# Kernel tuning notes

Hardware: AMD Instinct MI355X
Metric: run time of the kernel (lower is better)

The kernel has to match this reference:

```python
import jax, jax.numpy as jnp
import numpy as np

DIM = 768
HEADS = 12
HEAD_DIM = DIM // HEADS
EPS = 1e-5


def layernorm(x, gamma, beta):
    mu = jnp.mean(x, axis=-1, keepdims=True)
    var = jnp.var(x, axis=-1, keepdims=True)
    return (x - mu) * jax.lax.rsqrt(var + EPS) * gamma + beta


def setup_inputs() -> dict:
    key = jax.random.key(0)
    ks = jax.random.split(key, 9)
    B, N, C = 4, 2048, DIM
    s_in = 1.0 / np.sqrt(C)
    return {
        "x": jax.random.normal(ks[0], (B, N, C), dtype=jnp.float32),
        "qkv_w": jax.random.normal(ks[1], (3 * C, C), dtype=jnp.float32) * s_in,
        "qkv_b": jnp.zeros((3 * C,), dtype=jnp.float32),
        "proj_w": jax.random.normal(ks[2], (C, C), dtype=jnp.float32) * s_in,
        "proj_b": jnp.zeros((C,), dtype=jnp.float32),
        "q_gamma": jnp.ones((HEAD_DIM,), dtype=jnp.float32),
        "q_beta": jnp.zeros((HEAD_DIM,), dtype=jnp.float32),
        "k_gamma": jnp.ones((HEAD_DIM,), dtype=jnp.float32),
        "k_beta": jnp.zeros((HEAD_DIM,), dtype=jnp.float32),
    }


def reference(x, qkv_w, qkv_b, proj_w, proj_b, q_gamma, q_beta, k_gamma, k_beta):
    B, N, C = x.shape
    H, Dh = HEADS, C // HEADS
    scale = Dh ** (-0.5)
    # qkv projection: [B,N,3C] -> [3,B,H,N,Dh]
    qkv = (x @ qkv_w.T + qkv_b).reshape(B, N, 3, H, Dh).transpose(2, 0, 3, 1, 4)
    q, k, v = qkv[0], qkv[1], qkv[2]
    q = layernorm(q, q_gamma, q_beta)
    k = layernorm(k, k_gamma, k_beta)
    # explicit full score matrix [B,H,N,N] as in the original module
    attn = jnp.einsum("bhqd,bhkd->bhqk", q, k) * scale
    attn = jax.nn.softmax(attn, axis=-1)
    out = jnp.einsum("bhqk,bhkd->bhqd", attn, v)  # [B,H,N,Dh]
    out = out.transpose(0, 2, 1, 3).reshape(B, N, C)
    return out @ proj_w.T + proj_b
```

## Files before the change

### kernel.cpp

```cpp
#include <hip/hip_runtime.h>
#include <hip/hip_bf16.h>
#include <cstdint>
#include <cstddef>

#define BB 4
#define SEQ 2048
#define CD 768
#define NH 12
#define DH 64
#define MROWS (BB*SEQ)
#define NQKV (3*CD)

typedef float f32x4 __attribute__((ext_vector_type(4)));
typedef float f32x16 __attribute__((ext_vector_type(16)));
typedef short bf16x8 __attribute__((ext_vector_type(8)));

static __device__ __forceinline__ unsigned short f2bf(float f) {
  union { float f; unsigned int u; } cv; cv.f = f;
  unsigned int u = cv.u;
  unsigned int r = (u + 0x7FFFu + ((u >> 16) & 1u)) >> 16;
  return (unsigned short)r;
}

static __device__ __forceinline__ float fexp2(float x) {
#if __has_builtin(__builtin_amdgcn_exp2f)
  return __builtin_amdgcn_exp2f(x);
#else
  float r; asm("v_exp_f32 %0, %1" : "=v"(r) : "v"(x)); return r;
#endif
}

#define GAS __attribute__((address_space(1)))
#define LAS __attribute__((address_space(3)))
static __device__ __forceinline__ void gl2lds16(const void* g, void* l) {
  __builtin_amdgcn_global_load_lds((const GAS void*)g, (LAS void*)l, 16, 0, 0);
}

#define MFMA(a, b, c) __builtin_amdgcn_mfma_f32_16x16x32_bf16((a), (b), (c), 0, 0, 0)
#define MFMA32(a, b, c) __builtin_amdgcn_mfma_f32_32x32x16_bf16((a), (b), (c), 0, 0, 0)
#define PACKBF(dst, x, y) asm("v_cvt_pk_bf16_f32 %0, %1, %2" : "=v"(dst) : "v"(x), "v"(y))
#define SWAP32(a, b) asm("v_permlane32_swap_b32 %0, %1" : "+v"(a), "+v"(b))

#define QSC 0.18033688011112042f

__global__ __launch_bounds__(256) void cvt_bf16(const float* __restrict__ in,
                                                unsigned short* __restrict__ out, int n4) {
  int i = blockIdx.x * 256 + threadIdx.x;
  if (i >= n4) return;
  float4 v = reinterpret_cast<const float4*>(in)[i];
  unsigned int lo = (unsigned int)f2bf(v.x) | ((unsigned int)f2bf(v.y) << 16);
  unsigned int hi = (unsigned int)f2bf(v.z) | ((unsigned int)f2bf(v.w) << 16);
  reinterpret_cast<uint2*>(out)[i] = make_uint2(lo, hi);
}

__global__ __launch_bounds__(256) void qkv_gemm(
    const unsigned short* __restrict__ Xb, const unsigned short* __restrict__ Wb,
    const float* __restrict__ bias,
    const float* __restrict__ qg, const float* __restrict__ qbt,
    const float* __restrict__ kg, const float* __restrict__ kbt,
    unsigned short* __restrict__ Qo, unsigned short* __restrict__ Ko,
    unsigned short* __restrict__ Vt) {
  __shared__ unsigned short Als[2][128 * 64];
  __shared__ unsigned short Bls[2][128 * 64];
  const int tid = threadIdx.x;
  const int wid = tid >> 6, lane = tid & 63;
  const int g = lane >> 4, cl = lane & 15;
  const int wr = (wid >> 1) * 64, wc = (wid & 1) * 64;

  const int wg = blockIdx.x;
  const int wgid = (wg & 7) * 144 + (wg >> 3);
  const int bm = wgid / 18, bn = wgid % 18;

  f32x4 acc[4][4] = {};

  const int srow = tid >> 3;
  const int scol = ((tid & 7) ^ (srow & 7)) * 8;
  const unsigned short* Abase = Xb + (size_t)(bm * 128 + srow) * CD + scol;
  const unsigned short* Bbase = Wb + (size_t)(bn * 128 + srow) * CD + scol;

#define QSTG(buf, kt)                                                         \
  do {                                                                        \
    gl2lds16(Abase + (size_t)0 * 32 * CD + (kt) * 64, &Als[buf][0 * 2048 + tid * 8]); \
    gl2lds16(Abase + (size_t)1 * 32 * CD + (kt) * 64, &Als[buf][1 * 2048 + tid * 8]); \
    gl2lds16(Abase + (size_t)2 * 32 * CD + (kt) * 64, &Als[buf][2 * 2048 + tid * 8]); \
    gl2lds16(Abase + (size_t)3 * 32 * CD + (kt) * 64, &Als[buf][3 * 2048 + tid * 8]); \
    gl2lds16(Bbase + (size_t)0 * 32 * CD + (kt) * 64, &Bls[buf][0 * 2048 + tid * 8]); \
    gl2lds16(Bbase + (size_t)1 * 32 * CD + (kt) * 64, &Bls[buf][1 * 2048 + tid * 8]); \
    gl2lds16(Bbase + (size_t)2 * 32 * CD + (kt) * 64, &Bls[buf][2 * 2048 + tid * 8]); \
    gl2lds16(Bbase + (size_t)3 * 32 * CD + (kt) * 64, &Bls[buf][3 * 2048 + tid * 8]); \
  } while (0)

  QSTG(0, 0);
  __syncthreads();
  const int NKT = CD / 64;
  for (int kt = 0; kt < NKT; ++kt) {
    const int cur = kt & 1;
    if (kt + 1 < NKT) QSTG(cur ^ 1, kt + 1);
    bf16x8 bfr[4][2];
#pragma unroll
    for (int j = 0; j < 4; ++j) {
      const int Bcol = wc + j * 16 + cl;
      const int sw = (Bcol & 7) << 3;
      bfr[j][0] = *(const bf16x8*)&Bls[cur][Bcol * 64 + ((g * 8) ^ sw)];
      bfr[j][1] = *(const bf16x8*)&Bls[cur][Bcol * 64 + ((32 + g * 8) ^ sw)];
    }
    __builtin_amdgcn_s_setprio(1);
#pragma unroll
    for (int i = 0; i < 4; ++i) {
      const int Arow = wr + i * 16 + cl;
      const int sw = (Arow & 7) << 3;
      bf16x8 a0 = *(const bf16x8*)&Als[cur][Arow * 64 + ((g * 8) ^ sw)];
      bf16x8 a1 = *(const bf16x8*)&Als[cur][Arow * 64 + ((32 + g * 8) ^ sw)];
#pragma unroll
      for (int j = 0; j < 4; ++j) {
        acc[i][j] = MFMA(a0, bfr[j][0], acc[i][j]);
        acc[i][j] = MFMA(a1, bfr[j][1], acc[i][j]);
      }
    }
    __builtin_amdgcn_s_setprio(0);
    __syncthreads();
  }
#undef QSTG

  const int j0 = bn * 128 + wc;
  const int t = j0 / CD;
  const int h = (j0 % CD) / DH;
  float bia[4], gam[4] = {0, 0, 0, 0}, bet[4] = {0, 0, 0, 0};
#pragma unroll
  for (int j = 0; j < 4; ++j) {
    int d = j * 16 + cl;
    bia[j] = bias[j0 + d];
    if (t == 0) { gam[j] = qg[d] * QSC; bet[j] = qbt[d] * QSC; }
    else if (t == 1) { gam[j] = kg[d]; bet[j] = kbt[d]; }
  }

  if (t == 2) {
#pragma unroll
    for (int i = 0; i < 4; ++i) {
      const int mrow = bm * 128 + wr + i * 16 + g * 4;
      const int b = mrow >> 11, nn = mrow & 2047;
#pragma unroll
      for (int j = 0; j < 4; ++j) {
        const int d = j * 16 + cl;
        unsigned int lo = (unsigned int)f2bf(acc[i][j][0] + bia[j]) |
                          ((unsigned int)f2bf(acc[i][j][1] + bia[j]) << 16);
        unsigned int hi2 = (unsigned int)f2bf(acc[i][j][2] + bia[j]) |
                           ((unsigned int)f2bf(acc[i][j][3] + bia[j]) << 16);
        *reinterpret_cast<uint2*>(&Vt[((size_t)(b * NH + h) * DH + d) * SEQ + nn]) =
            make_uint2(lo, hi2);
      }
    }
    return;
  }

  unsigned short* Out = (t == 0) ? Qo : Ko;
#pragma unroll
  for (int i = 0; i < 4; ++i) {
#pragma unroll
    for (int r = 0; r < 4; ++r) {
      float vj[4];
#pragma unroll
      for (int j = 0; j < 4; ++j) vj[j] = acc[i][j][r] + bia[j];
      const int m = bm * 128 + wr + i * 16 + g * 4 + r;
      const int b = m >> 11, n = m & 2047;
      size_t base = ((size_t)(b * NH + h) * SEQ + n) * DH;
      float s = vj[0] + vj[1] + vj[2] + vj[3];
      float ss = vj[0] * vj[0] + vj[1] * vj[1] + vj[2] * vj[2] + vj[3] * vj[3];
#pragma unroll
      for (int msk = 1; msk < 16; msk <<= 1) {
        s += __shfl_xor(s, msk, 64);
        ss += __shfl_xor(ss, msk, 64);
      }
      float mu = s * (1.0f / 64.0f);
      float var = ss * (1.0f / 64.0f) - mu * mu;
      float rstd = rsqrtf(var + 1e-5f);
#pragma unroll
      for (int j = 0; j < 4; ++j)
        Out[base + j * 16 + cl] = f2bf((vj[j] - mu) * rstd * gam[j] + bet[j]);
    }
  }
}

__global__ __launch_bounds__(256, 3) void attn_fwd(
    const unsigned short* __restrict__ Qb, const unsigned short* __restrict__ Kb,
    const unsigned short* __restrict__ Vtb, unsigned short* __restrict__ Ob) {
  __shared__ unsigned short kl[2][64 * 64];
  __shared__ unsigned short vt[2][64 * 64];
  __shared__ float linv[4][32];
  const int tid = threadIdx.x, wave = tid >> 6, lane = tid & 63;
  const int q32 = lane & 31, hi = lane >> 5;

  const int wg = blockIdx.x;
  const int lin = (wg & 7) * 96 + (wg >> 3);
  const int bh = lin >> 4;
  const int qbase = (lin & 15) * 128 + wave * 32;

  const unsigned short* qrow = Qb + ((size_t)bh * SEQ + qbase + q32) * DH + hi * 8;
  bf16x8 qf[4];
#pragma unroll
  for (int dc = 0; dc < 4; ++dc) qf[dc] = *(const bf16x8*)&qrow[dc * 16];

  const unsigned short* Kh = Kb + (size_t)bh * SEQ * DH;
  const unsigned short* Vth = Vtb + (size_t)bh * DH * SEQ;

  const int sr = tid >> 3;
  const int sc = 8 * ((tid & 7) ^ (sr & 7));
  const int ksw = (q32 & 7) << 3;

#define ASTAGE(buf, kb0)                                                      \
  do {                                                                        \
    gl2lds16(&Kh[(size_t)((kb0) + sr) * DH + sc], &kl[buf][tid * 8]);         \
    gl2lds16(&Kh[(size_t)((kb0) + sr + 32) * DH + sc], &kl[buf][tid * 8 + 2048]); \
    gl2lds16(&Vth[(size_t)sr * SEQ + (kb0) + sc], &vt[buf][tid * 8]);         \
    gl2lds16(&Vth[(size_t)(sr + 32) * SEQ + (kb0) + sc], &vt[buf][tid * 8 + 2048]); \
  } while (0)

  f32x16 o0 = {}, o1 = {};
  float su0 = 0.0f, su1 = 0.0f, su2 = 0.0f, su3 = 0.0f;

  ASTAGE(0, 0);
  __syncthreads();
  const int NT = SEQ / 64;
#pragma unroll 2
  for (int it = 0; it < NT; ++it) {
    const int cur = it & 1;
    if (it + 1 < NT) ASTAGE(cur ^ 1, (it + 1) * 64);

    f32x16 s0 = {}, s1 = {};
    __builtin_amdgcn_s_setprio(1);
#pragma unroll
    for (int dc = 0; dc < 4; ++dc) {
      const int colb = dc * 16 + hi * 8;
      bf16x8 kf0 = *(const bf16x8*)&kl[cur][q32 * 64 + (colb ^ ksw)];
      bf16x8 kf1 = *(const bf16x8*)&kl[cur][(32 + q32) * 64 + (colb ^ ksw)];
      s0 = MFMA32(kf0, qf[dc], s0);
      s1 = MFMA32(kf1, qf[dc], s1);
    }
    __builtin_amdgcn_s_setprio(0);

#pragma unroll
    for (int r = 0; r < 16; r += 4) {
      s0[r + 0] = fexp2(s0[r + 0]); su0 += s0[r + 0];
      s0[r + 1] = fexp2(s0[r + 1]); su1 += s0[r + 1];
      s0[r + 2] = fexp2(s0[r + 2]); su2 += s0[r + 2];
      s0[r + 3] = fexp2(s0[r + 3]); su3 += s0[r + 3];
    }
#pragma unroll
    for (int r = 0; r < 16; r += 4) {
      s1[r + 0] = fexp2(s1[r + 0]); su0 += s1[r + 0];
      s1[r + 1] = fexp2(s1[r + 1]); su1 += s1[r + 1];
      s1[r + 2] = fexp2(s1[r + 2]); su2 += s1[r + 2];
      s1[r + 3] = fexp2(s1[r + 3]); su3 += s1[r + 3];
    }

    bf16x8 pav[4];
#pragma unroll
    for (int c = 0; c < 4; ++c) {
      const int b = 8 * (c & 1);
      unsigned int wA0, wA1, wB0, wB1;
      if (c < 2) {
        PACKBF(wA0, s0[b + 0], s0[b + 1]); PACKBF(wA1, s0[b + 2], s0[b + 3]);
        PACKBF(wB0, s0[b + 4], s0[b + 5]); PACKBF(wB1, s0[b + 6], s0[b + 7]);
      } else {
        PACKBF(wA0, s1[b + 0], s1[b + 1]); PACKBF(wA1, s1[b + 2], s1[b + 3]);
        PACKBF(wB0, s1[b + 4], s1[b + 5]); PACKBF(wB1, s1[b + 6], s1[b + 7]);
      }
      SWAP32(wA0, wB0);
      SWAP32(wA1, wB1);
      union { unsigned int w[4]; bf16x8 v; } u;
      u.w[0] = wA0; u.w[1] = wA1; u.w[2] = wB0; u.w[3] = wB1;
      pav[c] = u.v;
    }

    __builtin_amdgcn_s_setprio(1);
#pragma unroll
    for (int c = 0; c < 4; ++c) {
      const int colb = c * 16 + hi * 8;
      bf16x8 vf0 = *(const bf16x8*)&vt[cur][q32 * 64 + (colb ^ ksw)];
      bf16x8 vf1 = *(const bf16x8*)&vt[cur][(32 + q32) * 64 + (colb ^ ksw)];
      o0 = MFMA32(pav[c], vf0, o0);
      o1 = MFMA32(pav[c], vf1, o1);
    }
    __builtin_amdgcn_s_setprio(0);
    __syncthreads();
  }
#undef ASTAGE

  float lsum = (su0 + su1) + (su2 + su3);
  lsum += __shfl_xor(lsum, 32, 64);
  linv[wave][q32] = __builtin_amdgcn_rcpf(lsum);
  __syncthreads();

  const int b = bh / NH, h = bh % NH;
#pragma unroll
  for (int r = 0; r < 16; ++r) {
    const int qq = (r & 3) + 8 * (r >> 2) + 4 * hi;
    const float iv = linv[wave][qq];
    size_t base = ((size_t)(b * SEQ + qbase + qq)) * CD + h * DH;
    Ob[base + q32] = f2bf(o0[r] * iv);
    Ob[base + 32 + q32] = f2bf(o1[r] * iv);
  }
}

__global__ __launch_bounds__(256) void proj_gemm(
    const unsigned short* __restrict__ Ab, const unsigned short* __restrict__ Wb,
    const float* __restrict__ bias, float* __restrict__ out) {
  __shared__ unsigned short Als[2][128 * 64];
  __shared__ unsigned short Bls[2][128 * 64];
  const int tid = threadIdx.x;
  const int wid = tid >> 6, lane = tid & 63;
  const int g = lane >> 4, cl = lane & 15;
  const int bm = blockIdx.x, bn = blockIdx.y;
  const int wr = (wid >> 1) * 64, wc = (wid & 1) * 64;

  f32x4 acc[4][4] = {};

  const int srow = tid >> 3;
  const int scol = ((tid & 7) ^ (srow & 7)) * 8;
  const unsigned short* Abase = Ab + (size_t)(bm * 128 + srow) * CD + scol;
  const unsigned short* Bbase = Wb + (size_t)(bn * 128 + srow) * CD + scol;

#define PSTG(buf, kt)                                                         \
  do {                                                                        \
    gl2lds16(Abase + (size_t)0 * 32 * CD + (kt) * 64, &Als[buf][0 * 2048 + tid * 8]); \
    gl2lds16(Abase + (size_t)1 * 32 * CD + (kt) * 64, &Als[buf][1 * 2048 + tid * 8]); \
    gl2lds16(Abase + (size_t)2 * 32 * CD + (kt) * 64, &Als[buf][2 * 2048 + tid * 8]); \
    gl2lds16(Abase + (size_t)3 * 32 * CD + (kt) * 64, &Als[buf][3 * 2048 + tid * 8]); \
    gl2lds16(Bbase + (size_t)0 * 32 * CD + (kt) * 64, &Bls[buf][0 * 2048 + tid * 8]); \
    gl2lds16(Bbase + (size_t)1 * 32 * CD + (kt) * 64, &Bls[buf][1 * 2048 + tid * 8]); \
    gl2lds16(Bbase + (size_t)2 * 32 * CD + (kt) * 64, &Bls[buf][2 * 2048 + tid * 8]); \
    gl2lds16(Bbase + (size_t)3 * 32 * CD + (kt) * 64, &Bls[buf][3 * 2048 + tid * 8]); \
  } while (0)

  PSTG(0, 0);
  __syncthreads();
  const int NKT = CD / 64;
  for (int kt = 0; kt < NKT; ++kt) {
    const int cur = kt & 1;
    if (kt + 1 < NKT) PSTG(cur ^ 1, kt + 1);
    bf16x8 bfr[4][2];
#pragma unroll
    for (int j = 0; j < 4; ++j) {
      const int Bcol = wc + j * 16 + cl;
      const int sw = (Bcol & 7) << 3;
      bfr[j][0] = *(const bf16x8*)&Bls[cur][Bcol * 64 + ((g * 8) ^ sw)];
      bfr[j][1] = *(const bf16x8*)&Bls[cur][Bcol * 64 + ((32 + g * 8) ^ sw)];
    }
    __builtin_amdgcn_s_setprio(1);
#pragma unroll
    for (int i = 0; i < 4; ++i) {
      const int Arow = wr + i * 16 + cl;
      const int sw = (Arow & 7) << 3;
      bf16x8 a0 = *(const bf16x8*)&Als[cur][Arow * 64 + ((g * 8) ^ sw)];
      bf16x8 a1 = *(const bf16x8*)&Als[cur][Arow * 64 + ((32 + g * 8) ^ sw)];
#pragma unroll
      for (int j = 0; j < 4; ++j) {
        acc[i][j] = MFMA(a0, bfr[j][0], acc[i][j]);
        acc[i][j] = MFMA(a1, bfr[j][1], acc[i][j]);
      }
    }
    __builtin_amdgcn_s_setprio(0);
    __syncthreads();
  }
#undef PSTG

  const int j0 = bn * 128 + wc;
  float pb4[4];
#pragma unroll
  for (int j = 0; j < 4; ++j) pb4[j] = bias[j0 + j * 16 + cl];
#pragma unroll
  for (int i = 0; i < 4; ++i) {
#pragma unroll
    for (int r = 0; r < 4; ++r) {
      const int m = bm * 128 + wr + i * 16 + g * 4 + r;
      float* orow = out + (size_t)m * CD + j0;
#pragma unroll
      for (int j = 0; j < 4; ++j) orow[j * 16 + cl] = acc[i][j][r] + pb4[j];
    }
  }
}

extern "C" void kernel_launch(void* const* d_in, const int* in_sizes, int n_in,
                              void* d_out, int out_size, void* d_ws, size_t ws_size,
                              hipStream_t stream) {
  const float* x = (const float*)d_in[0];
  const float* qkv_w = (const float*)d_in[1];
  const float* qkv_b = (const float*)d_in[2];
  const float* proj_w = (const float*)d_in[3];
  const float* proj_b = (const float*)d_in[4];
  const float* q_gamma = (const float*)d_in[5];
  const float* q_beta = (const float*)d_in[6];
  const float* k_gamma = (const float*)d_in[7];
  const float* k_beta = (const float*)d_in[8];
  float* out = (float*)d_out;

  char* w = (char*)d_ws;
  unsigned short* Xb = (unsigned short*)w; w += (size_t)MROWS * CD * 2;
  unsigned short* Wq = (unsigned short*)w; w += (size_t)NQKV * CD * 2;
  unsigned short* Wp = (unsigned short*)w; w += (size_t)CD * CD * 2;
  unsigned short* Qo = (unsigned short*)w; w += (size_t)BB * NH * SEQ * DH * 2;
  unsigned short* Ko = (unsigned short*)w; w += (size_t)BB * NH * SEQ * DH * 2;
  unsigned short* Vt = (unsigned short*)w; w += (size_t)BB * NH * SEQ * DH * 2;
  unsigned short* Ob = (unsigned short*)w; w += (size_t)MROWS * CD * 2;

  cvt_bf16<<<MROWS * CD / 1024, 256, 0, stream>>>(x, Xb, MROWS * CD / 4);
  cvt_bf16<<<NQKV * CD / 1024, 256, 0, stream>>>(qkv_w, Wq, NQKV * CD / 4);
  cvt_bf16<<<CD * CD / 1024, 256, 0, stream>>>(proj_w, Wp, CD * CD / 4);

  qkv_gemm<<<(MROWS / 128) * (NQKV / 128), 256, 0, stream>>>(
      Xb, Wq, qkv_b, q_gamma, q_beta, k_gamma, k_beta, Qo, Ko, Vt);

  attn_fwd<<<SEQ / 128 * BB * NH, 256, 0, stream>>>(Qo, Ko, Vt, Ob);

  proj_gemm<<<dim3(MROWS / 128, CD / 128), 256, 0, stream>>>(Ob, Wp, proj_b, out);
}
```

Measured before the change: 145.2 us.

## Stage QKV GEMM epilogue through LDS for vectorized stores; merge bf16 conversions

The three fp32-to-bf16 conversion launches become one kernel that picks its source by index. The QKV GEMM epilogue now writes the accumulators to a swizzled LDS buffer. Each thread then reads a full 64-wide head row, computes LayerNorm serially and writes 16-byte bf16 stores; V^T is written with 16-byte stores along the sequence dimension. This replaces scattered 2-byte and 8-byte stores and the shuffle reductions, at the cost of an extra LDS round trip, a barrier, and 64-float register arrays per thread.

Result: faster. 133.8 us (-7.9%).

```diff
diff --git a/kernel.cpp b/kernel.cpp
--- a/kernel.cpp
+++ b/kernel.cpp
@@ -43,14 +43,25 @@
 
 #define QSC 0.18033688011112042f
 
-__global__ __launch_bounds__(256) void cvt_bf16(const float* __restrict__ in,
-                                                unsigned short* __restrict__ out, int n4) {
+#define CN1 (MROWS * CD / 4)
+#define CN2 (CN1 + NQKV * CD / 4)
+#define CN3 (CN2 + CD * CD / 4)
+__global__ __launch_bounds__(256) void cvt_all(
+    const float* __restrict__ x, const float* __restrict__ wq, const float* __restrict__ wp,
+    unsigned short* __restrict__ Xb, unsigned short* __restrict__ Wq,
+    unsigned short* __restrict__ Wp) {
   int i = blockIdx.x * 256 + threadIdx.x;
-  if (i >= n4) return;
-  float4 v = reinterpret_cast<const float4*>(in)[i];
+  if (i >= CN3) return;
+  const float* src;
+  unsigned short* dst;
+  int k;
+  if (i < CN1) { src = x; dst = Xb; k = i; }
+  else if (i < CN2) { src = wq; dst = Wq; k = i - CN1; }
+  else { src = wp; dst = Wp; k = i - CN2; }
+  float4 v = reinterpret_cast<const float4*>(src)[k];
   unsigned int lo = (unsigned int)f2bf(v.x) | ((unsigned int)f2bf(v.y) << 16);
   unsigned int hi = (unsigned int)f2bf(v.z) | ((unsigned int)f2bf(v.w) << 16);
-  reinterpret_cast<uint2*>(out)[i] = make_uint2(lo, hi);
+  reinterpret_cast<uint2*>(dst)[k] = make_uint2(lo, hi);
 }
 
 __global__ __launch_bounds__(256) void qkv_gemm(
@@ -60,8 +71,9 @@
     const float* __restrict__ kg, const float* __restrict__ kbt,
     unsigned short* __restrict__ Qo, unsigned short* __restrict__ Ko,
     unsigned short* __restrict__ Vt) {
-  __shared__ unsigned short Als[2][128 * 64];
-  __shared__ unsigned short Bls[2][128 * 64];
+  __shared__ unsigned short smem[4 * 128 * 64];
+#define ALS(buf) (&smem[(buf) * 8192])
+#define BLS(buf) (&smem[16384 + (buf) * 8192])
   const int tid = threadIdx.x;
   const int wid = tid >> 6, lane = tid & 63;
   const int g = lane >> 4, cl = lane & 15;
@@ -80,14 +92,14 @@
 
 #define QSTG(buf, kt)                                                         \
   do {                                                                        \
-    gl2lds16(Abase + (size_t)0 * 32 * CD + (kt) * 64, &Als[buf][0 * 2048 + tid * 8]); \
-    gl2lds16(Abase + (size_t)1 * 32 * CD + (kt) * 64, &Als[buf][1 * 2048 + tid * 8]); \
-    gl2lds16(Abase + (size_t)2 * 32 * CD + (kt) * 64, &Als[buf][2 * 2048 + tid * 8]); \
-    gl2lds16(Abase + (size_t)3 * 32 * CD + (kt) * 64, &Als[buf][3 * 2048 + tid * 8]); \
-    gl2lds16(Bbase + (size_t)0 * 32 * CD + (kt) * 64, &Bls[buf][0 * 2048 + tid * 8]); \
-    gl2lds16(Bbase + (size_t)1 * 32 * CD + (kt) * 64, &Bls[buf][1 * 2048 + tid * 8]); \
-    gl2lds16(Bbase + (size_t)2 * 32 * CD + (kt) * 64, &Bls[buf][2 * 2048 + tid * 8]); \
-    gl2lds16(Bbase + (size_t)3 * 32 * CD + (kt) * 64, &Bls[buf][3 * 2048 + tid * 8]); \
+    gl2lds16(Abase + (size_t)0 * 32 * CD + (kt) * 64, ALS(buf) + 0 * 2048 + tid * 8); \
+    gl2lds16(Abase + (size_t)1 * 32 * CD + (kt) * 64, ALS(buf) + 1 * 2048 + tid * 8); \
+    gl2lds16(Abase + (size_t)2 * 32 * CD + (kt) * 64, ALS(buf) + 2 * 2048 + tid * 8); \
+    gl2lds16(Abase + (size_t)3 * 32 * CD + (kt) * 64, ALS(buf) + 3 * 2048 + tid * 8); \
+    gl2lds16(Bbase + (size_t)0 * 32 * CD + (kt) * 64, BLS(buf) + 0 * 2048 + tid * 8); \
+    gl2lds16(Bbase + (size_t)1 * 32 * CD + (kt) * 64, BLS(buf) + 1 * 2048 + tid * 8); \
+    gl2lds16(Bbase + (size_t)2 * 32 * CD + (kt) * 64, BLS(buf) + 2 * 2048 + tid * 8); \
+    gl2lds16(Bbase + (size_t)3 * 32 * CD + (kt) * 64, BLS(buf) + 3 * 2048 + tid * 8); \
   } while (0)
 
   QSTG(0, 0);
@@ -101,16 +113,16 @@
     for (int j = 0; j < 4; ++j) {
       const int Bcol = wc + j * 16 + cl;
       const int sw = (Bcol & 7) << 3;
-      bfr[j][0] = *(const bf16x8*)&Bls[cur][Bcol * 64 + ((g * 8) ^ sw)];
-      bfr[j][1] = *(const bf16x8*)&Bls[cur][Bcol * 64 + ((32 + g * 8) ^ sw)];
+      bfr[j][0] = *(const bf16x8*)&BLS(cur)[Bcol * 64 + ((g * 8) ^ sw)];
+      bfr[j][1] = *(const bf16x8*)&BLS(cur)[Bcol * 64 + ((32 + g * 8) ^ sw)];
     }
     __builtin_amdgcn_s_setprio(1);
 #pragma unroll
     for (int i = 0; i < 4; ++i) {
       const int Arow = wr + i * 16 + cl;
       const int sw = (Arow & 7) << 3;
-      bf16x8 a0 = *(const bf16x8*)&Als[cur][Arow * 64 + ((g * 8) ^ sw)];
-      bf16x8 a1 = *(const bf16x8*)&Als[cur][Arow * 64 + ((32 + g * 8) ^ sw)];
+      bf16x8 a0 = *(const bf16x8*)&ALS(cur)[Arow * 64 + ((g * 8) ^ sw)];
+      bf16x8 a1 = *(const bf16x8*)&ALS(cur)[Arow * 64 + ((32 + g * 8) ^ sw)];
 #pragma unroll
       for (int j = 0; j < 4; ++j) {
         acc[i][j] = MFMA(a0, bfr[j][0], acc[i][j]);
@@ -122,63 +134,94 @@
   }
 #undef QSTG
 
-  const int j0 = bn * 128 + wc;
-  const int t = j0 / CD;
-  const int h = (j0 % CD) / DH;
-  float bia[4], gam[4] = {0, 0, 0, 0}, bet[4] = {0, 0, 0, 0};
-#pragma unroll
-  for (int j = 0; j < 4; ++j) {
-    int d = j * 16 + cl;
-    bia[j] = bias[j0 + d];
-    if (t == 0) { gam[j] = qg[d] * QSC; bet[j] = qbt[d] * QSC; }
-    else if (t == 1) { gam[j] = kg[d]; bet[j] = kbt[d]; }
-  }
+  float* cb = (float*)smem;
+#define CIDX(r, c) ((r) * 128 + (((((c) >> 2)) ^ ((r) & 31)) << 2) + ((c) & 3))
+#pragma unroll
+  for (int i = 0; i < 4; ++i)
+#pragma unroll
+    for (int j = 0; j < 4; ++j)
+#pragma unroll
+      for (int r = 0; r < 4; ++r)
+        cb[CIDX(wr + i * 16 + g * 4 + r, wc + j * 16 + cl)] = acc[i][j][r];
+  __syncthreads();
+
+  const int t = bn / 6;
+  const int h0 = (bn % 6) * 2;
+  const int j0 = bn * 128;
 
   if (t == 2) {
-#pragma unroll
-    for (int i = 0; i < 4; ++i) {
-      const int mrow = bm * 128 + wr + i * 16 + g * 4;
-      const int b = mrow >> 11, nn = mrow & 2047;
-#pragma unroll
-      for (int j = 0; j < 4; ++j) {
-        const int d = j * 16 + cl;
-        unsigned int lo = (unsigned int)f2bf(acc[i][j][0] + bia[j]) |
-                          ((unsigned int)f2bf(acc[i][j][1] + bia[j]) << 16);
-        unsigned int hi2 = (unsigned int)f2bf(acc[i][j][2] + bia[j]) |
-                           ((unsigned int)f2bf(acc[i][j][3] + bia[j]) << 16);
-        *reinterpret_cast<uint2*>(&Vt[((size_t)(b * NH + h) * DH + d) * SEQ + nn]) =
-            make_uint2(lo, hi2);
-      }
+    const int col = tid >> 1, nh = tid & 1;
+    const int h = h0 + (col >> 6), d = col & 63;
+    const float bia = bias[j0 + col];
+    const int m0 = bm * 128;
+    const int b = m0 >> 11;
+    const int nn0 = (m0 & 2047) + nh * 64;
+    unsigned short* dst = &Vt[((size_t)(b * NH + h) * DH + d) * SEQ + nn0];
+#pragma unroll
+    for (int k8 = 0; k8 < 8; ++k8) {
+      union { unsigned short us[8]; uint4 v; } u;
+#pragma unroll
+      for (int e = 0; e < 8; ++e)
+        u.us[e] = f2bf(cb[CIDX(nh * 64 + k8 * 8 + e, col)] + bia);
+      *reinterpret_cast<uint4*>(&dst[k8 * 8]) = u.v;
     }
     return;
   }
 
-  unsigned short* Out = (t == 0) ? Qo : Ko;
-#pragma unroll
-  for (int i = 0; i < 4; ++i) {
-#pragma unroll
-    for (int r = 0; r < 4; ++r) {
-      float vj[4];
-#pragma unroll
-      for (int j = 0; j < 4; ++j) vj[j] = acc[i][j][r] + bia[j];
-      const int m = bm * 128 + wr + i * 16 + g * 4 + r;
-      const int b = m >> 11, n = m & 2047;
-      size_t base = ((size_t)(b * NH + h) * SEQ + n) * DH;
-      float s = vj[0] + vj[1] + vj[2] + vj[3];
-      float ss = vj[0] * vj[0] + vj[1] * vj[1] + vj[2] * vj[2] + vj[3] * vj[3];
-#pragma unroll
-      for (int msk = 1; msk < 16; msk <<= 1) {
-        s += __shfl_xor(s, msk, 64);
-        ss += __shfl_xor(ss, msk, 64);
-      }
-      float mu = s * (1.0f / 64.0f);
-      float var = ss * (1.0f / 64.0f) - mu * mu;
-      float rstd = rsqrtf(var + 1e-5f);
-#pragma unroll
-      for (int j = 0; j < 4; ++j)
-        Out[base + j * 16 + cl] = f2bf((vj[j] - mu) * rstd * gam[j] + bet[j]);
-    }
-  }
+  const int nl = tid >> 1, half = tid & 1;
+  const int h = h0 + half;
+  const int m = bm * 128 + nl;
+  const int b = m >> 11, n = m & 2047;
+  const float* gmp = (t == 0) ? qg : kg;
+  const float* btp = (t == 0) ? qbt : kbt;
+  const float sc = (t == 0) ? QSC : 1.0f;
+  const float* bi = bias + j0 + half * 64;
+
+  float v[64];
+#pragma unroll
+  for (int k4 = 0; k4 < 16; ++k4) {
+    f32x4 q = *(const f32x4*)&cb[nl * 128 + ((((half * 16 + k4)) ^ (nl & 31)) << 2)];
+    float4 b4 = reinterpret_cast<const float4*>(bi)[k4];
+    v[k4 * 4 + 0] = q[0] + b4.x;
+    v[k4 * 4 + 1] = q[1] + b4.y;
+    v[k4 * 4 + 2] = q[2] + b4.z;
+    v[k4 * 4 + 3] = q[3] + b4.w;
+  }
+  float s0 = 0, s1 = 0, s2 = 0, s3 = 0, q0 = 0, q1 = 0, q2 = 0, q3 = 0;
+#pragma unroll
+  for (int k = 0; k < 64; k += 4) {
+    s0 += v[k]; q0 += v[k] * v[k];
+    s1 += v[k + 1]; q1 += v[k + 1] * v[k + 1];
+    s2 += v[k + 2]; q2 += v[k + 2] * v[k + 2];
+    s3 += v[k + 3]; q3 += v[k + 3] * v[k + 3];
+  }
+  const float sum = (s0 + s1) + (s2 + s3);
+  const float ssum = (q0 + q1) + (q2 + q3);
+  const float mu = sum * (1.0f / 64.0f);
+  const float var = ssum * (1.0f / 64.0f) - mu * mu;
+  const float rstd = rsqrtf(var + 1e-5f);
+
+  unsigned short* dst = ((t == 0) ? Qo : Ko) + ((size_t)(b * NH + h) * SEQ + n) * DH;
+#pragma unroll
+  for (int k8 = 0; k8 < 8; ++k8) {
+    float4 gm4 = reinterpret_cast<const float4*>(gmp)[k8 * 2];
+    float4 gm4b = reinterpret_cast<const float4*>(gmp)[k8 * 2 + 1];
+    float4 bt4 = reinterpret_cast<const float4*>(btp)[k8 * 2];
+    float4 bt4b = reinterpret_cast<const float4*>(btp)[k8 * 2 + 1];
+    const float* g8 = &gm4.x;
+    const float* b8 = &bt4.x;
+    union { unsigned short us[8]; uint4 vv; } u;
+#pragma unroll
+    for (int e = 0; e < 4; ++e) {
+      u.us[e] = f2bf(((v[k8 * 8 + e] - mu) * rstd * (&gm4.x)[e] + (&bt4.x)[e]) * sc);
+      u.us[4 + e] = f2bf(((v[k8 * 8 + 4 + e] - mu) * rstd * (&gm4b.x)[e] + (&bt4b.x)[e]) * sc);
+    }
+    (void)g8; (void)b8;
+    *reinterpret_cast<uint4*>(&dst[k8 * 8]) = u.vv;
+  }
+#undef CIDX
+#undef ALS
+#undef BLS
 }
 
 __global__ __launch_bounds__(256, 3) void attn_fwd(
@@ -403,9 +446,7 @@
   unsigned short* Vt = (unsigned short*)w; w += (size_t)BB * NH * SEQ * DH * 2;
   unsigned short* Ob = (unsigned short*)w; w += (size_t)MROWS * CD * 2;
 
-  cvt_bf16<<<MROWS * CD / 1024, 256, 0, stream>>>(x, Xb, MROWS * CD / 4);
-  cvt_bf16<<<NQKV * CD / 1024, 256, 0, stream>>>(qkv_w, Wq, NQKV * CD / 4);
-  cvt_bf16<<<CD * CD / 1024, 256, 0, stream>>>(proj_w, Wp, CD * CD / 4);
+  cvt_all<<<(CN3 + 255) / 256, 256, 0, stream>>>(x, qkv_w, proj_w, Xb, Wq, Wp);
 
   qkv_gemm<<<(MROWS / 128) * (NQKV / 128), 256, 0, stream>>>(
       Xb, Wq, qkv_b, q_gamma, q_beta, k_gamma, k_beta, Qo, Ko, Vt);
```
